# Kernel tuning notes

Measured on AMD Instinct MI355X. Metric: run time of the kernel, lower is better.

The kernel has to match this reference:

```python
import jax, jax.numpy as jnp
import numpy as np

# ---- static config (mirrors cfg) ----
B, N, K = 2, 8192, 40
FIRST_DL = 0.03
CONV_RADIUS = 2.5
DEFORM_RADIUS = 5.0
ARCH = ['simple', 'resnetb', 'resnetb_strided', 'resnetb', 'resnetb_strided', 'resnetb', 'nearest_upsample']
SENTINEL = N  # out-of-range support index (torch code uses N_spts_total; here per-batch padded slot count)
GRID = 4096   # voxel hash multiplier; coords stay < GRID for pts in [0,1], dl >= 0.06


def _ball_query_one(q, s, qmask, smask, radius):
    """Radius ball-query: K nearest supports within radius. q:[N,3] s:[M,3]."""
    d2 = jnp.sum((q[:, None, :] - s[None, :, :]) ** 2, axis=-1)          # [N,M]
    d2 = jnp.where(smask[None, :] & (d2 <= radius * radius), d2, jnp.inf)
    vals, idx = jax.lax.top_k(-d2, K)                                     # [N,K]
    idx = jnp.where(jnp.isfinite(vals) & qmask[:, None], idx, SENTINEL)
    return idx.astype(jnp.int32)


ball_query = jax.vmap(_ball_query_one, in_axes=(0, 0, 0, 0, None))


def _grid_subsample_one(pts, mask, dl):
    """Voxel-grid subsampling with unweighted average (padded to N rows)."""
    INT_MAX = jnp.iinfo(jnp.int32).max
    c = jnp.floor(pts / dl).astype(jnp.int32)                             # nonneg for pts in [0,1]
    key_v = (c[:, 0] * GRID + c[:, 1]) * GRID + c[:, 2]
    key_v = jnp.where(mask, key_v, INT_MAX)
    order = jnp.argsort(key_v)
    sk = key_v[order]
    sp = pts[order]
    new = jnp.concatenate([jnp.ones((1,), bool), sk[1:] != sk[:-1]])
    seg = jnp.cumsum(new) - 1                                             # segment id per sorted point
    sums = jax.ops.segment_sum(sp, seg, num_segments=N)                   # [N,3]
    cnt = jax.ops.segment_sum(jnp.ones((N,), pts.dtype), seg, num_segments=N)
    segkey = jax.ops.segment_max(sk, seg, num_segments=N)
    valid = (cnt > 0) & (segkey != INT_MAX)                               # invalid pads sort last
    means = jnp.where(valid[:, None], sums / jnp.maximum(cnt, 1.0)[:, None], 0.0)
    return means, valid, jnp.sum(valid).astype(jnp.int32)


grid_subsample = jax.vmap(_grid_subsample_one, in_axes=(0, 0, None))


def setup_inputs() -> dict:
    key = jax.random.key(0)
    pts = jax.random.uniform(key, (B, N, 3), dtype=jnp.float32)
    return {"pts": pts}


def reference(pts):
    pmask = jnp.ones((B, N), bool)
    lengths = jnp.full((B,), N, jnp.int32)
    points = pts
    r_normal = FIRST_DL * CONV_RADIUS
    layer_blocks = []
    out_points, out_neigh, out_pool, out_up, out_len = [], [], [], [], []
    for bi, block in enumerate(ARCH):
        if 'global' in block or 'upsample' in block:
            break
        if not ('pool' in block or 'strided' in block):
            layer_blocks.append(block)
            if bi < len(ARCH) - 1 and 'upsample' not in ARCH[bi + 1]:
                continue
        if layer_blocks:
            if any('deformable' in b for b in layer_blocks[:-1]):
                r = r_normal * DEFORM_RADIUS / CONV_RADIUS
            else:
                r = r_normal
            conv_i = ball_query(points, points, pmask, pmask, r)
        else:
            conv_i = jnp.full((B, N, K), SENTINEL, jnp.int32)
        if 'pool' in block or 'strided' in block:
            dl = 2 * r_normal / CONV_RADIUS
            pool_p, pool_m, pool_len = grid_subsample(points, pmask, dl)
            r = r_normal * DEFORM_RADIUS / CONV_RADIUS if 'deformable' in block else r_normal
            pool_i = ball_query(pool_p, points, pool_m, pmask, r)
            up_i = ball_query(points, pool_p, pmask, pool_m, 2 * r)
        else:
            pool_i = jnp.full((B, N, K), SENTINEL, jnp.int32)
            up_i = jnp.full((B, N, K), SENTINEL, jnp.int32)
            pool_p = jnp.zeros((B, N, 3), points.dtype)
            pool_m = jnp.zeros((B, N), bool)
            pool_len = jnp.zeros((B,), jnp.int32)
        out_points.append(points)
        out_neigh.append(conv_i)
        out_pool.append(pool_i)
        out_up.append(up_i)
        out_len.append(lengths)
        points, pmask, lengths = pool_p, pool_m, pool_len
        r_normal *= 2
        layer_blocks = []
    return (jnp.stack(out_points),   # [L,B,N,3] padded points per layer
            jnp.stack(out_neigh),    # [L,B,N,K] conv neighbor indices
            jnp.stack(out_pool),     # [L,B,N,K] pooling indices
            jnp.stack(out_up),       # [L,B,N,K] upsampling indices
            jnp.stack(out_len))      # [L,B]     valid lengths
```

## Files before the change

kernel.cpp:

```cpp
#include <hip/hip_runtime.h>

#define BB   2
#define NN   8192
#define KNN  40
#define SENT 8192
#define G0   17
#define G1   9
#define G0_3 (G0*G0*G0)
#define G1_3 (G1*G1*G1)

#define GA   13
#define GB   6
#define GC   3
#define GA_3 (GA*GA*GA)
#define GB_3 (GB*GB*GB)
#define GC_3 (GC*GC*GC)

typedef unsigned long long ull;
typedef unsigned int       u32;
typedef unsigned short     u16;

__device__ __forceinline__ float sqdist(float qx, float qy, float qz,
                                        float sx, float sy, float sz) {
    float dx = __fsub_rn(qx, sx);
    float dy = __fsub_rn(qy, sy);
    float dz = __fsub_rn(qz, sz);
    return __fadd_rn(__fadd_rn(__fmul_rn(dx, dx), __fmul_rn(dy, dy)),
                     __fmul_rn(dz, dz));
}

__device__ __forceinline__ int cell1(float p, float Gf, int G) {
    int c = (int)floorf(__fmul_rn(p, Gf));
    return min(max(c, 0), G - 1);
}
__device__ __forceinline__ int vcell1(float p, float dlf, int G) {
    int c = (int)floorf(__fdiv_rn(p, dlf));
    return min(max(c, 0), G - 1);
}

__device__ __forceinline__ ull shfl_u64(ull x, int src) {
    int lo = __shfl((int)(u32)x, src);
    int hi = __shfl((int)(u32)(x >> 32), src);
    return ((ull)(u32)hi << 32) | (ull)(u32)lo;
}
__device__ __forceinline__ ull shflxor_u64(ull x, int m) {
    int lo = __shfl_xor((int)(u32)x, m);
    int hi = __shfl_xor((int)(u32)(x >> 32), m);
    return ((ull)(u32)hi << 32) | (ull)(u32)lo;
}

__global__ void prep_kernel(const float* __restrict__ pts, float* __restrict__ dout) {
    const size_t PN = (size_t)BB * NN * 3;
    const size_t IN = (size_t)BB * NN * KNN;
    float* out_points0 = dout;
    float* out_pool2   = dout + 3 * PN + 3 * IN + 2 * IN;
    float* out_up2     = dout + 3 * PN + 6 * IN + 2 * IN;
    float* out_len     = dout + 3 * PN + 9 * IN;
    int i = blockIdx.x * 256 + threadIdx.x;
    if (i < (int)PN) out_points0[i] = pts[i];
    if (i < (int)IN) {
        out_pool2[i] = (float)SENT;
        out_up2[i]   = (float)SENT;
    }
    if (i == 0) { out_len[0] = (float)NN; out_len[1] = (float)NN; }
}

__global__ __launch_bounds__(1024) void csr_build(
    const float* __restrict__ pts, const int* __restrict__ len_ptr, int len_const,
    int G, int G3, int* __restrict__ off, float4* __restrict__ lst4,
    float dlfv, int Gv, int G3v, int* __restrict__ offv, int* __restrict__ rankv,
    int* __restrict__ lstv, int* __restrict__ lenv_dev, float* __restrict__ lenv_out_f) {
    __shared__ int scnt[GA_3];
    __shared__ int soff[GA_3];
    __shared__ int svcnt[G0_3];
    __shared__ int svoff[G0_3];
    __shared__ int wsum[16];
    int b = blockIdx.x;
    int t = threadIdx.x;
    int len = len_ptr ? len_ptr[b] : len_const;
    const float* pb = pts + (size_t)b * NN * 3;
    float Gf = (float)G;
    bool dosub = Gv > 0;
    for (int v = t; v < G3; v += 1024) scnt[v] = 0;
    if (dosub) for (int v = t; v < G3v; v += 1024) svcnt[v] = 0;
    __syncthreads();
    for (int i = t; i < len; i += 1024) {
        float px = pb[i * 3], py = pb[i * 3 + 1], pz = pb[i * 3 + 2];
        int c = (cell1(px, Gf, G) * G + cell1(py, Gf, G)) * G + cell1(pz, Gf, G);
        atomicAdd(&scnt[c], 1);
        if (dosub) {
            int cv = (vcell1(px, dlfv, Gv) * Gv + vcell1(py, dlfv, Gv)) * Gv
                     + vcell1(pz, dlfv, Gv);
            atomicAdd(&svcnt[cv], 1);
        }
    }
    __syncthreads();
    int lane = t & 63, wid = t >> 6;
    {
        int per = (G3 + 1023) >> 10;
        int start = t * per, end = min(start + per, G3);
        if (start > G3) start = G3;
        int csum = 0;
        for (int v = start; v < end; ++v) csum += scnt[v];
        int inc = csum;
        for (int d = 1; d < 64; d <<= 1) {
            int u = __shfl_up(inc, d);
            if (lane >= d) inc += u;
        }
        if (lane == 63) wsum[wid] = inc;
        __syncthreads();
        if (t < 16) {
            int wv = wsum[t];
            for (int d = 1; d < 16; d <<= 1) {
                int u = __shfl_up(wv, d);
                if (t >= d) wv += u;
            }
            wsum[t] = wv;
        }
        __syncthreads();
        int excl = inc - csum + (wid ? wsum[wid - 1] : 0);
        int run = excl;
        int* offb = off + (size_t)b * (G3 + 1);
        for (int v = start; v < end; ++v) {
            soff[v] = run;
            offb[v] = run;
            run += scnt[v];
        }
        if (t == 0) offb[G3] = len;
    }
    __syncthreads();
    if (dosub) {
        int per = (G3v + 1023) >> 10;
        int start = t * per, end = min(start + per, G3v);
        if (start > G3v) start = G3v;
        int ce = 0, co = 0;
        for (int v = start; v < end; ++v) { ce += svcnt[v]; co += (svcnt[v] > 0); }
        int pack = (ce << 14) | co;
        int inc = pack;
        for (int d = 1; d < 64; d <<= 1) {
            int u = __shfl_up(inc, d);
            if (lane >= d) inc += u;
        }
        if (lane == 63) wsum[wid] = inc;
        __syncthreads();
        if (t < 16) {
            int wv = wsum[t];
            for (int d = 1; d < 16; d <<= 1) {
                int u = __shfl_up(wv, d);
                if (t >= d) wv += u;
            }
            wsum[t] = wv;
        }
        __syncthreads();
        int excl = inc - pack + (wid ? wsum[wid - 1] : 0);
        int rune = excl >> 14;
        int runo = excl & 16383;
        int total = wsum[15] & 16383;
        int* offvb  = offv  + (size_t)b * (G3v + 1);
        int* rankvb = rankv + (size_t)b * G3v;
        for (int v = start; v < end; ++v) {
            svoff[v]  = rune;
            offvb[v]  = rune;
            rankvb[v] = runo;
            rune += svcnt[v];
            runo += (svcnt[v] > 0);
        }
        if (t == 0) {
            offvb[G3v] = len;
            lenv_dev[b] = total;
            lenv_out_f[b] = (float)total;
        }
    }
    __syncthreads();
    for (int v = t; v < G3; v += 1024) scnt[v] = 0;
    if (dosub) for (int v = t; v < G3v; v += 1024) svcnt[v] = 0;
    __syncthreads();
    float4* lst4b = lst4 + (size_t)b * NN;
    int* lstvb = dosub ? (lstv + (size_t)b * NN) : nullptr;
    for (int i = t; i < len; i += 1024) {
        float px = pb[i * 3], py = pb[i * 3 + 1], pz = pb[i * 3 + 2];
        int c = (cell1(px, Gf, G) * G + cell1(py, Gf, G)) * G + cell1(pz, Gf, G);
        int pos = soff[c] + atomicAdd(&scnt[c], 1);
        lst4b[pos] = make_float4(px, py, pz, __int_as_float(i));
        if (dosub) {
            int cv = (vcell1(px, dlfv, Gv) * Gv + vcell1(py, dlfv, Gv)) * Gv
                     + vcell1(pz, dlfv, Gv);
            int posv = svoff[cv] + atomicAdd(&svcnt[cv], 1);
            lstvb[posv] = i;
        }
    }
}

struct BqArgs {
    const float* q; const int* qlp; int qlc;
    const float4* lst; const int* off;
    int G; int G3; float r2; float* out;
};
struct MeansArgs {
    const float* pts; const int* off; const int* rnk; const int* lst;
    const int* len_dev; int G3; float* out;
};

__global__ __launch_bounds__(256) void bq_fused(BqArgs pA, BqArgs pB, BqArgs pC,
                                                MeansArgs pM, int nbq) {
    const ull INITK = ~0ull;
    __shared__ ull wlds[4][512];
    int z = blockIdx.z;
    if (z >= nbq) {
        int b = blockIdx.y;
        int i = blockIdx.x * 256 + threadIdx.x;
        if (i >= NN) return;
        const float* pb = pM.pts + (size_t)b * NN * 3;
        const int* offb = pM.off + (size_t)b * (pM.G3 + 1);
        const int* lstb = pM.lst + (size_t)b * NN;
        if (i < pM.G3) {
            int s = offb[i], e = offb[i + 1];
            int cn = e - s;
            if (cn > 0) {
                float sx = 0.f, sy = 0.f, sz = 0.f;
                int last = -1;
                for (int k = 0; k < cn; ++k) {
                    int m = 0x7FFFFFFF;
                    for (int j = s; j < e; ++j) {
                        int idx = lstb[j];
                        if (idx > last && idx < m) m = idx;
                    }
                    sx = __fadd_rn(sx, pb[m * 3]);
                    sy = __fadd_rn(sy, pb[m * 3 + 1]);
                    sz = __fadd_rn(sz, pb[m * 3 + 2]);
                    last = m;
                }
                float rinv = __frcp_rn((float)cn);
                int rk = pM.rnk[(size_t)b * pM.G3 + i];
                float* op = pM.out + ((size_t)b * NN + rk) * 3;
                op[0] = __fmul_rn(sx, rinv);
                op[1] = __fmul_rn(sy, rinv);
                op[2] = __fmul_rn(sz, rinv);
            }
        }
        int total = pM.len_dev[blockIdx.y];
        if (i >= total) {
            float* op = pM.out + ((size_t)blockIdx.y * NN + i) * 3;
            op[0] = 0.f; op[1] = 0.f; op[2] = 0.f;
        }
        return;
    }
    const float* qpts   = z == 0 ? pA.q   : (z == 1 ? pB.q   : pC.q);
    const int* qlen_ptr = z == 0 ? pA.qlp : (z == 1 ? pB.qlp : pC.qlp);
    int qlen_const      = z == 0 ? pA.qlc : (z == 1 ? pB.qlc : pC.qlc);
    const float4* lst   = z == 0 ? pA.lst : (z == 1 ? pB.lst : pC.lst);
    const int* off      = z == 0 ? pA.off : (z == 1 ? pB.off : pC.off);
    int G               = z == 0 ? pA.G   : (z == 1 ? pB.G   : pC.G);
    int G3              = z == 0 ? pA.G3  : (z == 1 ? pB.G3  : pC.G3);
    float r2            = z == 0 ? pA.r2  : (z == 1 ? pB.r2  : pC.r2);
    float* out          = z == 0 ? pA.out : (z == 1 ? pB.out : pC.out);

    int t = threadIdx.x;
    int lane = t & 63;
    ull* wl = wlds[t >> 6];
    int b = blockIdx.y;
    int qi = blockIdx.x * 4 + (t >> 6);
    int qlen = qlen_ptr ? qlen_ptr[b] : qlen_const;
    float* op = out + ((size_t)b * NN + qi) * KNN;
    if (qi >= qlen) {
        if (lane < KNN) op[lane] = (float)SENT;
        return;
    }
    const float* qp = qpts + ((size_t)b * NN + qi) * 3;
    float qx = qp[0], qy = qp[1], qz = qp[2];
    float Gf = (float)G;
    int cx = cell1(qx, Gf, G), cy = cell1(qy, Gf, G), cz = cell1(qz, Gf, G);
    const int* offb = off + (size_t)b * (G3 + 1);
    const float4* lstb = lst + (size_t)b * NN;

    int cnt = 0, cst = 0;
    if (lane < 27) {
        int dz = lane % 3 - 1, dy = (lane / 3) % 3 - 1, dxx = lane / 9 - 1;
        int x = cx + dxx, y = cy + dy, zz = cz + dz;
        bool ok = ((unsigned)x < (unsigned)G) & ((unsigned)y < (unsigned)G)
                                              & ((unsigned)zz < (unsigned)G);
        int c = ok ? (x * G + y) * G + zz : 0;
        int s = ok ? offb[c] : 0;
        int e = ok ? offb[c + 1] : 0;
        cnt = e - s;
        cst = s;
    }
    int incl = cnt;
#pragma unroll
    for (int d_ = 1; d_ < 64; d_ <<= 1) {
        int u = __shfl_up(incl, d_);
        if (lane >= d_) incl += u;
    }
    int excl = incl - cnt;
    int T = __shfl(incl, 63);

    ull res = INITK;
    bool have_res = false;
    for (int r0 = 0; r0 < T; r0 += 512) {
        ull c0 = INITK, c1 = INITK, c2 = INITK, c3 = INITK,
            c4 = INITK, c5 = INITK, c6 = INITK, c7 = INITK;
#define FILL(S, CS) if (r0 + (S) * 64 < T) {                                   \
            int g = r0 + (S) * 64 + lane;                                      \
            bool gok = g < T;                                                  \
            int gc = gok ? g : (T - 1);                                        \
            int d = 0;                                                         \
            if (__shfl(excl, d | 16) <= gc) d |= 16;                           \
            if (__shfl(excl, d | 8)  <= gc) d |= 8;                            \
            if (__shfl(excl, d | 4)  <= gc) d |= 4;                            \
            if (__shfl(excl, d | 2)  <= gc) d |= 2;                            \
            if (__shfl(excl, d | 1)  <= gc) d |= 1;                            \
            int st = __shfl(cst, d), eg = __shfl(excl, d);                     \
            float4 f = lstb[st + (gc - eg)];                                   \
            float d2 = sqdist(qx, qy, qz, f.x, f.y, f.z);                      \
            if (gok && d2 <= r2)                                               \
                CS = (((ull)__float_as_uint(d2)) << 13)                        \
                     | (ull)(u32)__float_as_int(f.w);                          \
        }
        FILL(0, c0) FILL(1, c1) FILL(2, c2) FILL(3, c3)
        FILL(4, c4) FILL(5, c5) FILL(6, c6) FILL(7, c7)
#undef FILL
#define CE(A, B) { ull lo_ = (A < B) ? A : B; ull hi_ = (A < B) ? B : A; A = lo_; B = hi_; }
        CE(c0,c1) CE(c2,c3) CE(c4,c5) CE(c6,c7)
        CE(c0,c2) CE(c1,c3) CE(c4,c6) CE(c5,c7)
        CE(c1,c2) CE(c5,c6)
        CE(c0,c4) CE(c1,c5) CE(c2,c6) CE(c3,c7)
        CE(c2,c4) CE(c3,c5)
        CE(c1,c2) CE(c3,c4) CE(c5,c6)
#undef CE
        int m = (c0 != INITK) + (c1 != INITK) + (c2 != INITK) + (c3 != INITK)
              + (c4 != INITK) + (c5 != INITK) + (c6 != INITK) + (c7 != INITK);
        int incm = m;
#pragma unroll
        for (int d_ = 1; d_ < 64; d_ <<= 1) {
            int u = __shfl_up(incm, d_);
            if (lane >= d_) incm += u;
        }
        int base = incm - m;
        int M = __shfl(incm, 63);
        asm volatile("s_waitcnt lgkmcnt(0)" ::: "memory");
        __builtin_amdgcn_sched_barrier(0);
        if (m > 0) {
            wl[base] = c0;
            if (m > 1) wl[base + 1] = c1;
            if (m > 2) wl[base + 2] = c2;
            if (m > 3) wl[base + 3] = c3;
            if (m > 4) wl[base + 4] = c4;
            if (m > 5) wl[base + 5] = c5;
            if (m > 6) wl[base + 6] = c6;
            if (m > 7) wl[base + 7] = c7;
        }
        asm volatile("s_waitcnt lgkmcnt(0)" ::: "memory");
        __builtin_amdgcn_sched_barrier(0);
        int npass = (M + 63) >> 6;
        for (int p = 0; p < npass; ++p) {
            int D = p * 64 + lane;
            ull key = (D < M) ? wl[D] : INITK;
            int mc = M - p * 64;
#define BSTAGE(K) { _Pragma("unroll")                                          \
            for (int jj = (K) >> 1; jj > 0; jj >>= 1) {                        \
                ull other = shflxor_u64(key, jj);                              \
                bool up = ((lane & (K)) == 0);                                 \
                bool lowlane = ((lane & jj) == 0);                             \
                bool takeMin = (lowlane == up);                                \
                bool lt = key < other;                                         \
                key = (takeMin == lt) ? key : other;                           \
            } }
            if (mc > 1)  BSTAGE(2)
            if (mc > 2)  BSTAGE(4)
            if (mc > 4)  BSTAGE(8)
            if (mc > 8)  BSTAGE(16)
            if (mc > 16) BSTAGE(32)
            if (mc > 32) BSTAGE(64)
#undef BSTAGE
            if (!have_res) {
                res = key;
                have_res = true;
            } else {
                ull rb = shfl_u64(key, 63 - lane);
                ull lo_ = (res < rb) ? res : rb;
#pragma unroll
                for (int jj = 32; jj > 0; jj >>= 1) {
                    ull other = shflxor_u64(lo_, jj);
                    bool lowlane = ((lane & jj) == 0);
                    bool lt = lo_ < other;
                    lo_ = (lowlane == lt) ? lo_ : other;
                }
                res = lo_;
            }
        }
    }
    if (lane < KNN)
        op[lane] = (res == INITK) ? (float)SENT : (float)(int)(res & 0x1FFFu);
}

extern "C" void kernel_launch(void* const* d_in, const int* in_sizes, int n_in,
                              void* d_out, int out_size, void* d_ws, size_t ws_size,
                              hipStream_t stream) {
    const float* pts = (const float*)d_in[0];
    float* dout = (float*)d_out;
    const size_t PN = (size_t)BB * NN * 3;
    const size_t IN = (size_t)BB * NN * KNN;
    float* out_points = dout;
    float* out_neigh  = dout + 3 * PN;
    float* out_pool   = out_neigh + 3 * IN;
    float* out_up     = out_pool + 3 * IN;
    float* out_len    = out_up + 3 * IN;
    float* pts1 = out_points + PN;
    float* pts2 = out_points + 2 * PN;

    float4* lst4A = (float4*)d_ws;
    float4* lst4B = lst4A + (size_t)BB * NN;
    float4* lst4C = lst4B + (size_t)BB * NN;
    int*   len1  = (int*)(lst4C + (size_t)BB * NN);
    int*   len2  = len1 + BB;
    int*   offV0 = len2 + BB;
    int*   rnk0  = offV0 + (size_t)BB * (G0_3 + 1);
    int*   lstV0 = rnk0 + (size_t)BB * G0_3;
    int*   offV1 = lstV0 + (size_t)BB * NN;
    int*   rnk1  = offV1 + (size_t)BB * (G1_3 + 1);
    int*   lstV1 = rnk1 + (size_t)BB * G1_3;
    int*   offA  = lstV1 + (size_t)BB * NN;
    int*   offB  = offA + (size_t)BB * (GA_3 + 1);
    int*   offC  = offB + (size_t)BB * (GB_3 + 1);

    double r_normal = 0.03 * 2.5;
    double r0 = r_normal;
    double dl0 = 2.0 * r_normal / 2.5;
    float r2_0   = (float)(r0 * r0);
    float r2_up0 = (float)((2.0 * r0) * (2.0 * r0));
    float dlf0   = (float)dl0;
    r_normal *= 2.0;
    double r1 = r_normal;
    double dl1 = 2.0 * r_normal / 2.5;
    float r2_1   = (float)(r1 * r1);
    float r2_up1 = (float)((2.0 * r1) * (2.0 * r1));
    float dlf1   = (float)dl1;
    r_normal *= 2.0;
    float r2_2 = (float)(r_normal * r_normal);

    BqArgs conv0 = { pts,  nullptr, NN, lst4A, offA, GA, GA_3, r2_0,   out_neigh + 0 * IN };
    BqArgs pool0 = { pts1, len1,    0,  lst4A, offA, GA, GA_3, r2_0,   out_pool  + 0 * IN };
    BqArgs up0   = { pts,  nullptr, NN, lst4B, offB, GB, GB_3, r2_up0, out_up    + 0 * IN };
    BqArgs conv1 = { pts1, len1,    0,  lst4B, offB, GB, GB_3, r2_1,   out_neigh + 1 * IN };
    BqArgs pool1 = { pts2, len2,    0,  lst4B, offB, GB, GB_3, r2_1,   out_pool  + 1 * IN };
    BqArgs up1   = { pts1, len1,    0,  lst4C, offC, GC, GC_3, r2_up1, out_up    + 1 * IN };
    BqArgs conv2 = { pts2, len2,    0,  lst4C, offC, GC, GC_3, r2_2,   out_neigh + 2 * IN };
    MeansArgs means0 = { pts,  offV0, rnk0, lstV0, len1, G0_3, pts1 };
    MeansArgs means1 = { pts1, offV1, rnk1, lstV1, len2, G1_3, pts2 };

    dim3 gD1(NN / 4, BB, 2);
    dim3 gD2(NN / 4, BB, 4);
    dim3 gD3(NN / 4, BB, 3);

    prep_kernel<<<(int)((IN + 255) / 256), 256, 0, stream>>>(pts, dout);
    csr_build<<<BB, 1024, 0, stream>>>(pts, nullptr, NN, GA, GA_3, offA, lst4A,
                                       dlf0, G0, G0_3, offV0, rnk0, lstV0,
                                       len1, out_len + 2);
    bq_fused<<<gD1, 256, 0, stream>>>(conv0, conv0, conv0, means0, 1);
    csr_build<<<BB, 1024, 0, stream>>>(pts1, len1, 0, GB, GB_3, offB, lst4B,
                                       dlf1, G1, G1_3, offV1, rnk1, lstV1,
                                       len2, out_len + 4);
    bq_fused<<<gD2, 256, 0, stream>>>(pool0, up0, conv1, means1, 3);
    csr_build<<<BB, 1024, 0, stream>>>(pts2, len2, 0, GC, GC_3, offC, lst4C,
                                       0.f, 0, 0, nullptr, nullptr, nullptr,
                                       nullptr, nullptr);
    bq_fused<<<gD3, 256, 0, stream>>>(pool1, up1, conv2, means1, 3);
}
```

Before: 179.5 us.

## Move cell histogramming out of single-block CSR build into wide producer kernels

The per-batch CSR build ran on only two 1024-thread blocks, and its cell-counting pass over all points was serial per block. The histogram is now built with global atomics in the wide prep kernel for layer 0, and in the means branch of the fused ball-query kernel for later layers, which count the subsampled points as they are produced. The CSR kernel only loads the counts, scans and scatters. Separately, the ball-query candidate compaction drops the 8-element sorting network and uses a validity bitmask with popcount to place entries. The cost is an extra memset, global atomic contention, and more coupling between kernels.

```diff
diff --git a/kernel.cpp b/kernel.cpp
--- a/kernel.cpp
+++ b/kernel.cpp
@@ -49,7 +49,9 @@
     return ((ull)(u32)hi << 32) | (ull)(u32)lo;
 }
 
-__global__ void prep_kernel(const float* __restrict__ pts, float* __restrict__ dout) {
+__global__ void prep_kernel(const float* __restrict__ pts, float* __restrict__ dout,
+                            int* __restrict__ cntA, int* __restrict__ cntV0,
+                            float dlf0) {
     const size_t PN = (size_t)BB * NN * 3;
     const size_t IN = (size_t)BB * NN * KNN;
     float* out_points0 = dout;
@@ -62,13 +64,26 @@
         out_pool2[i] = (float)SENT;
         out_up2[i]   = (float)SENT;
     }
+    if (i < BB * NN) {
+        int b = i >> 13;
+        float px = pts[(size_t)i * 3], py = pts[(size_t)i * 3 + 1],
+              pz = pts[(size_t)i * 3 + 2];
+        const float Gf = (float)GA;
+        int c = (cell1(px, Gf, GA) * GA + cell1(py, Gf, GA)) * GA + cell1(pz, Gf, GA);
+        atomicAdd(&cntA[(size_t)b * GA_3 + c], 1);
+        int cv = (vcell1(px, dlf0, G0) * G0 + vcell1(py, dlf0, G0)) * G0
+                 + vcell1(pz, dlf0, G0);
+        atomicAdd(&cntV0[(size_t)b * G0_3 + cv], 1);
+    }
     if (i == 0) { out_len[0] = (float)NN; out_len[1] = (float)NN; }
 }
 
-__global__ __launch_bounds__(1024) void csr_build(
+__global__ __launch_bounds__(1024) void scan_scatter(
     const float* __restrict__ pts, const int* __restrict__ len_ptr, int len_const,
-    int G, int G3, int* __restrict__ off, float4* __restrict__ lst4,
-    float dlfv, int Gv, int G3v, int* __restrict__ offv, int* __restrict__ rankv,
+    int G, int G3, const int* __restrict__ cntg,
+    int* __restrict__ off, float4* __restrict__ lst4,
+    float dlfv, int Gv, int G3v, const int* __restrict__ cntvg,
+    int* __restrict__ offv, int* __restrict__ rankv,
     int* __restrict__ lstv, int* __restrict__ lenv_dev, float* __restrict__ lenv_out_f) {
     __shared__ int scnt[GA_3];
     __shared__ int soff[GA_3];
@@ -81,19 +96,8 @@
     const float* pb = pts + (size_t)b * NN * 3;
     float Gf = (float)G;
     bool dosub = Gv > 0;
-    for (int v = t; v < G3; v += 1024) scnt[v] = 0;
-    if (dosub) for (int v = t; v < G3v; v += 1024) svcnt[v] = 0;
-    __syncthreads();
-    for (int i = t; i < len; i += 1024) {
-        float px = pb[i * 3], py = pb[i * 3 + 1], pz = pb[i * 3 + 2];
-        int c = (cell1(px, Gf, G) * G + cell1(py, Gf, G)) * G + cell1(pz, Gf, G);
-        atomicAdd(&scnt[c], 1);
-        if (dosub) {
-            int cv = (vcell1(px, dlfv, Gv) * Gv + vcell1(py, dlfv, Gv)) * Gv
-                     + vcell1(pz, dlfv, Gv);
-            atomicAdd(&svcnt[cv], 1);
-        }
-    }
+    for (int v = t; v < G3; v += 1024) scnt[v] = cntg[(size_t)b * G3 + v];
+    if (dosub) for (int v = t; v < G3v; v += 1024) svcnt[v] = cntvg[(size_t)b * G3v + v];
     __syncthreads();
     int lane = t & 63, wid = t >> 6;
     {
@@ -199,6 +203,8 @@
 struct MeansArgs {
     const float* pts; const int* off; const int* rnk; const int* lst;
     const int* len_dev; int G3; float* out;
+    int Gc; int Gc3; int* cntc;
+    float dlv; int Gv; int Gv3; int* cntv;
 };
 
 __global__ __launch_bounds__(256) void bq_fused(BqArgs pA, BqArgs pB, BqArgs pC,
@@ -231,16 +237,27 @@
                     last = m;
                 }
                 float rinv = __frcp_rn((float)cn);
+                float mx = __fmul_rn(sx, rinv);
+                float my = __fmul_rn(sy, rinv);
+                float mz = __fmul_rn(sz, rinv);
                 int rk = pM.rnk[(size_t)b * pM.G3 + i];
                 float* op = pM.out + ((size_t)b * NN + rk) * 3;
-                op[0] = __fmul_rn(sx, rinv);
-                op[1] = __fmul_rn(sy, rinv);
-                op[2] = __fmul_rn(sz, rinv);
+                op[0] = mx; op[1] = my; op[2] = mz;
+                float Gcf = (float)pM.Gc;
+                int cc = (cell1(mx, Gcf, pM.Gc) * pM.Gc + cell1(my, Gcf, pM.Gc))
+                         * pM.Gc + cell1(mz, Gcf, pM.Gc);
+                atomicAdd(&pM.cntc[(size_t)b * pM.Gc3 + cc], 1);
+                if (pM.Gv > 0) {
+                    int cv = (vcell1(mx, pM.dlv, pM.Gv) * pM.Gv
+                              + vcell1(my, pM.dlv, pM.Gv)) * pM.Gv
+                             + vcell1(mz, pM.dlv, pM.Gv);
+                    atomicAdd(&pM.cntv[(size_t)b * pM.Gv3 + cv], 1);
+                }
             }
         }
-        int total = pM.len_dev[blockIdx.y];
+        int total = pM.len_dev[b];
         if (i >= total) {
-            float* op = pM.out + ((size_t)blockIdx.y * NN + i) * 3;
+            float* op = pM.out + ((size_t)b * NN + i) * 3;
             op[0] = 0.f; op[1] = 0.f; op[2] = 0.f;
         }
         return;
@@ -299,6 +316,7 @@
     for (int r0 = 0; r0 < T; r0 += 512) {
         ull c0 = INITK, c1 = INITK, c2 = INITK, c3 = INITK,
             c4 = INITK, c5 = INITK, c6 = INITK, c7 = INITK;
+        u32 vm = 0;
 #define FILL(S, CS) if (r0 + (S) * 64 < T) {                                   \
             int g = r0 + (S) * 64 + lane;                                      \
             bool gok = g < T;                                                  \
@@ -312,23 +330,16 @@
             int st = __shfl(cst, d), eg = __shfl(excl, d);                     \
             float4 f = lstb[st + (gc - eg)];                                   \
             float d2 = sqdist(qx, qy, qz, f.x, f.y, f.z);                      \
-            if (gok && d2 <= r2)                                               \
+            if (gok && d2 <= r2) {                                             \
                 CS = (((ull)__float_as_uint(d2)) << 13)                        \
                      | (ull)(u32)__float_as_int(f.w);                          \
+                vm |= (1u << (S));                                             \
+            }                                                                  \
         }
         FILL(0, c0) FILL(1, c1) FILL(2, c2) FILL(3, c3)
         FILL(4, c4) FILL(5, c5) FILL(6, c6) FILL(7, c7)
 #undef FILL
-#define CE(A, B) { ull lo_ = (A < B) ? A : B; ull hi_ = (A < B) ? B : A; A = lo_; B = hi_; }
-        CE(c0,c1) CE(c2,c3) CE(c4,c5) CE(c6,c7)
-        CE(c0,c2) CE(c1,c3) CE(c4,c6) CE(c5,c7)
-        CE(c1,c2) CE(c5,c6)
-        CE(c0,c4) CE(c1,c5) CE(c2,c6) CE(c3,c7)
-        CE(c2,c4) CE(c3,c5)
-        CE(c1,c2) CE(c3,c4) CE(c5,c6)
-#undef CE
-        int m = (c0 != INITK) + (c1 != INITK) + (c2 != INITK) + (c3 != INITK)
-              + (c4 != INITK) + (c5 != INITK) + (c6 != INITK) + (c7 != INITK);
+        int m = __popc(vm);
         int incm = m;
 #pragma unroll
         for (int d_ = 1; d_ < 64; d_ <<= 1) {
@@ -339,16 +350,14 @@
         int M = __shfl(incm, 63);
         asm volatile("s_waitcnt lgkmcnt(0)" ::: "memory");
         __builtin_amdgcn_sched_barrier(0);
-        if (m > 0) {
-            wl[base] = c0;
-            if (m > 1) wl[base + 1] = c1;
-            if (m > 2) wl[base + 2] = c2;
-            if (m > 3) wl[base + 3] = c3;
-            if (m > 4) wl[base + 4] = c4;
-            if (m > 5) wl[base + 5] = c5;
-            if (m > 6) wl[base + 6] = c6;
-            if (m > 7) wl[base + 7] = c7;
-        }
+        if (vm & 1u)   wl[base]                      = c0;
+        if (vm & 2u)   wl[base + __popc(vm & 1u)]    = c1;
+        if (vm & 4u)   wl[base + __popc(vm & 3u)]    = c2;
+        if (vm & 8u)   wl[base + __popc(vm & 7u)]    = c3;
+        if (vm & 16u)  wl[base + __popc(vm & 15u)]   = c4;
+        if (vm & 32u)  wl[base + __popc(vm & 31u)]   = c5;
+        if (vm & 64u)  wl[base + __popc(vm & 63u)]   = c6;
+        if (vm & 128u) wl[base + __popc(vm & 127u)]  = c7;
         asm volatile("s_waitcnt lgkmcnt(0)" ::: "memory");
         __builtin_amdgcn_sched_barrier(0);
         int npass = (M + 63) >> 6;
@@ -422,6 +431,12 @@
     int*   offA  = lstV1 + (size_t)BB * NN;
     int*   offB  = offA + (size_t)BB * (GA_3 + 1);
     int*   offC  = offB + (size_t)BB * (GB_3 + 1);
+    int*   cntA  = offC + (size_t)BB * (GC_3 + 1);
+    int*   cntV0 = cntA + (size_t)BB * GA_3;
+    int*   cntB  = cntV0 + (size_t)BB * G0_3;
+    int*   cntV1 = cntB + (size_t)BB * GB_3;
+    int*   cntC  = cntV1 + (size_t)BB * G1_3;
+    size_t cntBytes = (size_t)BB * (GA_3 + G0_3 + GB_3 + G1_3 + GC_3) * sizeof(int);
 
     double r_normal = 0.03 * 2.5;
     double r0 = r_normal;
@@ -445,24 +460,29 @@
     BqArgs pool1 = { pts2, len2,    0,  lst4B, offB, GB, GB_3, r2_1,   out_pool  + 1 * IN };
     BqArgs up1   = { pts1, len1,    0,  lst4C, offC, GC, GC_3, r2_up1, out_up    + 1 * IN };
     BqArgs conv2 = { pts2, len2,    0,  lst4C, offC, GC, GC_3, r2_2,   out_neigh + 2 * IN };
-    MeansArgs means0 = { pts,  offV0, rnk0, lstV0, len1, G0_3, pts1 };
-    MeansArgs means1 = { pts1, offV1, rnk1, lstV1, len2, G1_3, pts2 };
+    MeansArgs means0 = { pts,  offV0, rnk0, lstV0, len1, G0_3, pts1,
+                         GB, GB_3, cntB, dlf1, G1, G1_3, cntV1 };
+    MeansArgs means1 = { pts1, offV1, rnk1, lstV1, len2, G1_3, pts2,
+                         GC, GC_3, cntC, 0.f, 0, 0, nullptr };
 
     dim3 gD1(NN / 4, BB, 2);
     dim3 gD2(NN / 4, BB, 4);
     dim3 gD3(NN / 4, BB, 3);
 
-    prep_kernel<<<(int)((IN + 255) / 256), 256, 0, stream>>>(pts, dout);
-    csr_build<<<BB, 1024, 0, stream>>>(pts, nullptr, NN, GA, GA_3, offA, lst4A,
-                                       dlf0, G0, G0_3, offV0, rnk0, lstV0,
-                                       len1, out_len + 2);
+    hipMemsetAsync(cntA, 0, cntBytes, stream);
+    prep_kernel<<<(int)((IN + 255) / 256), 256, 0, stream>>>(pts, dout, cntA,
+                                                             cntV0, dlf0);
+    scan_scatter<<<BB, 1024, 0, stream>>>(pts, nullptr, NN, GA, GA_3, cntA,
+                                          offA, lst4A, dlf0, G0, G0_3, cntV0,
+                                          offV0, rnk0, lstV0, len1, out_len + 2);
     bq_fused<<<gD1, 256, 0, stream>>>(conv0, conv0, conv0, means0, 1);
-    csr_build<<<BB, 1024, 0, stream>>>(pts1, len1, 0, GB, GB_3, offB, lst4B,
-                                       dlf1, G1, G1_3, offV1, rnk1, lstV1,
-                                       len2, out_len + 4);
+    scan_scatter<<<BB, 1024, 0, stream>>>(pts1, len1, 0, GB, GB_3, cntB,
+                                          offB, lst4B, dlf1, G1, G1_3, cntV1,
+                                          offV1, rnk1, lstV1, len2, out_len + 4);
     bq_fused<<<gD2, 256, 0, stream>>>(pool0, up0, conv1, means1, 3);
-    csr_build<<<BB, 1024, 0, stream>>>(pts2, len2, 0, GC, GC_3, offC, lst4C,
-                                       0.f, 0, 0, nullptr, nullptr, nullptr,
-                                       nullptr, nullptr);
+    scan_scatter<<<BB, 1024, 0, stream>>>(pts2, len2, 0, GC, GC_3, cntC,
+                                          offC, lst4C, 0.f, 0, 0, nullptr,
+                                          nullptr, nullptr, nullptr, nullptr,
+                                          nullptr);
     bq_fused<<<gD3, 256, 0, stream>>>(pool1, up1, conv2, means1, 3);
 }
```

Result: slower. 186.8 us (+4.0%).
